# Kernel tuning notes

Hardware: AMD Instinct MI355X
Metric: run time of the kernel (lower is better)

Reference implementation:

```python
import jax, jax.numpy as jnp
import numpy as np

N_LOC = 20000
N_EXP = 200000
H = 64
E = 1500000
L = 400000


def setup_inputs() -> dict:
    key = jax.random.key(0)
    ks = jax.random.split(key, 24)
    f = jnp.float32
    w = lambda k, shp: jax.random.normal(k, shp, dtype=f) * 0.1
    # edges: ('location','of','experts'): src in [0,N_LOC), dst in [0,N_EXP)
    src = jax.random.randint(ks[0], (E,), 0, N_LOC)
    dst = jax.random.randint(ks[1], (E,), 0, N_EXP)
    edge_of = jnp.stack([src, dst])          # location -> experts
    edge_rev = jnp.stack([dst, src])         # experts -> location (ToUndirected)
    row = jax.random.randint(ks[2], (L,), 0, N_LOC)
    col = jax.random.randint(ks[3], (L,), 0, N_EXP)
    edge_label_index = jnp.stack([row, col])
    return dict(
        emb_loc=w(ks[4], (N_LOC, H)), emb_exp=w(ks[5], (N_EXP, H)),
        W1l_of=w(ks[6], (H, H)), b1_of=jnp.zeros((H,), f), W1r_of=w(ks[7], (H, H)),
        W1l_rev=w(ks[8], (H, H)), b1_rev=jnp.zeros((H,), f), W1r_rev=w(ks[9], (H, H)),
        W2l_of=w(ks[10], (H, H)), b2_of=jnp.zeros((H,), f), W2r_of=w(ks[11], (H, H)),
        W2l_rev=w(ks[12], (H, H)), b2_rev=jnp.zeros((H,), f), W2r_rev=w(ks[13], (H, H)),
        dW1=w(ks[14], (2 * H, H)), db1=jnp.zeros((H,), f),
        dW2=w(ks[15], (H, 1)), db2=jnp.zeros((1,), f),
        edge_of=edge_of, edge_rev=edge_rev, edge_label_index=edge_label_index,
    )


def _sage(x_src, x_dst, edge, Wl, b, Wr, n_dst):
    # PyG SAGEConv: lin_l(mean of neighbor msgs) + lin_r(x_dst); bias only in lin_l
    s, d = edge[0], edge[1]
    msg = x_src[s]                                   # [E, H] gather
    summed = jax.ops.segment_sum(msg, d, num_segments=n_dst)
    cnt = jax.ops.segment_sum(jnp.ones((edge.shape[1],), x_src.dtype), d, num_segments=n_dst)
    agg = summed / jnp.maximum(cnt, 1.0)[:, None]
    return agg @ Wl + b + x_dst @ Wr


def reference(emb_loc, emb_exp,
              W1l_of, b1_of, W1r_of, W1l_rev, b1_rev, W1r_rev,
              W2l_of, b2_of, W2r_of, W2l_rev, b2_rev, W2r_rev,
              dW1, db1, dW2, db2,
              edge_of, edge_rev, edge_label_index):
    # layer 1 (to_hetero: one conv per edge type; each dst type has one incoming type)
    z_exp = jax.nn.relu(_sage(emb_loc, emb_exp, edge_of, W1l_of, b1_of, W1r_of, N_EXP))
    z_loc = jax.nn.relu(_sage(emb_exp, emb_loc, edge_rev, W1l_rev, b1_rev, W1r_rev, N_LOC))
    # layer 2 (no relu)
    z_exp2 = _sage(z_loc, z_exp, edge_of, W2l_of, b2_of, W2r_of, N_EXP)
    z_loc2 = _sage(z_exp, z_loc, edge_rev, W2l_rev, b2_rev, W2r_rev, N_LOC)
    # EdgeDecoder: gather-concat-MLP
    row, col = edge_label_index[0], edge_label_index[1]
    z = jnp.concatenate([z_loc2[row], z_exp2[col]], axis=-1)  # [L, 2H]
    h = jax.nn.relu(z @ dW1 + db1)
    out = (h @ dW2 + db2).reshape(-1)
    return out
```

## Files before the change

### kernel.cpp

```cpp
#include <hip/hip_runtime.h>

#define H 64
#define NE 1500000
#define NLOC 20000
#define NEXP 200000
#define NL 400000
#define PAD_E 32
#define PAD_L 128

#define EB 896
#define NBE 224
#define LB 112
#define NBL 179
#define BIN_CHUNK 2048
#define NBIN ((NE + BIN_CHUNK - 1) / BIN_CHUNK)
#define EBSLOT 28
#define LBSLOT 32
#define ECAP 8192
#define LCAP 10240
#define FCAP 4096

#define WS_NEED 90546112ULL

typedef int vint4 __attribute__((ext_vector_type(4)));
typedef _Float16 f16x8 __attribute__((ext_vector_type(8)));
typedef float f32x4 __attribute__((ext_vector_type(4)));
typedef unsigned int u32;
typedef unsigned short u16;
typedef unsigned long long u64;

__device__ __forceinline__ float bcastf(float v, int k) {
  return __int_as_float(__builtin_amdgcn_readlane(__float_as_int(v), k));
}
__device__ __forceinline__ int bcasti(int v, int k) {
  return __builtin_amdgcn_readlane(v, k);
}

__global__ __launch_bounds__(256) void bin_kernel(
    const int* __restrict__ src, const int* __restrict__ dst,
    u32* __restrict__ expQ, u32* __restrict__ locQ,
    int* __restrict__ qcnt, int* __restrict__ flbk_cnt,
    u64* __restrict__ flbkQ)
{
  __shared__ u32 eb[NBE * EBSLOT];
  __shared__ u32 lb[NBL * LBSLOT];
  __shared__ int ec[NBE], lc[NBL], ebase[NBE], lbase[NBL];

  const int tid = threadIdx.x;
  for (int i = tid; i < NBE; i += 256) ec[i] = 0;
  for (int i = tid; i < NBL; i += 256) lc[i] = 0;
  __syncthreads();

  const long base = (long)blockIdx.x * BIN_CHUNK + tid * 8;
  if (base < NE) {
    vint4 s0 = __builtin_nontemporal_load((const vint4*)(src + base));
    vint4 s1 = __builtin_nontemporal_load((const vint4*)(src + base + 4));
    vint4 d0 = __builtin_nontemporal_load((const vint4*)(dst + base));
    vint4 d1 = __builtin_nontemporal_load((const vint4*)(dst + base + 4));
    int ss[8] = {s0.x, s0.y, s0.z, s0.w, s1.x, s1.y, s1.z, s1.w};
    int dd[8] = {d0.x, d0.y, d0.z, d0.w, d1.x, d1.y, d1.z, d1.w};
#pragma unroll
    for (int k = 0; k < 8; k++) {
      const u32 d = (u32)dd[k], s = (u32)ss[k];
      {
        const u32 b = d / (u32)EB;
        const int pos = atomicAdd(&ec[b], 1);
        if (pos < EBSLOT) {
          eb[b * EBSLOT + pos] = ((d - b * EB) << 16) | s;
        } else {
          int fi = atomicAdd(flbk_cnt, 1);
          if (fi < FCAP) flbkQ[fi] = ((u64)d << 32) | (u64)s;
        }
      }
      {
        const u32 b = s / (u32)LB;
        const int pos = atomicAdd(&lc[b], 1);
        if (pos < LBSLOT) {
          lb[b * LBSLOT + pos] = ((s - b * LB) << 18) | d;
        } else {
          int fi = atomicAdd(flbk_cnt, 1);
          if (fi < FCAP) flbkQ[fi] = (1ULL << 63) | ((u64)s << 32) | (u64)d;
        }
      }
    }
  }
  __syncthreads();

  for (int i = tid; i < NBE; i += 256) {
    const int c = min(ec[i], EBSLOT);
    ebase[i] = c ? atomicAdd(&qcnt[i], c) : 0;
  }
  for (int i = tid; i < NBL; i += 256) {
    const int c = min(lc[i], LBSLOT);
    lbase[i] = c ? atomicAdd(&qcnt[NBE + i], c) : 0;
  }
  __syncthreads();

  const int wid = tid >> 6, ln = tid & 63;
  for (int b = wid; b < NBE; b += 4) {
    const int c = min(ec[b], EBSLOT);
    if (ln < c) {
      const int idx = ebase[b] + ln;
      const u32 r = eb[b * EBSLOT + ln];
      if (idx < ECAP) {
        expQ[(long)b * ECAP + idx] = r;
      } else {
        int fi = atomicAdd(flbk_cnt, 1);
        if (fi < FCAP)
          flbkQ[fi] = ((u64)(b * EB + (r >> 16)) << 32) | (u64)(r & 0xFFFF);
      }
    }
  }
  for (int b = wid; b < NBL; b += 4) {
    const int c = min(lc[b], LBSLOT);
    if (ln < c) {
      const int idx = lbase[b] + ln;
      const u32 r = lb[b * LBSLOT + ln];
      if (idx < LCAP) {
        locQ[(long)b * LCAP + idx] = r;
      } else {
        int fi = atomicAdd(flbk_cnt, 1);
        if (fi < FCAP)
          flbkQ[fi] = (1ULL << 63) | ((u64)(b * LB + (r >> 18)) << 32) |
                      (u64)(r & 0x3FFFF);
      }
    }
  }
}

__global__ __launch_bounds__(256) void build_kernel(
    const u32* __restrict__ expQ, const u32* __restrict__ locQ,
    const int* __restrict__ qcnt,
    u16* __restrict__ nbr_exp, int* __restrict__ nbr_loc,
    int* __restrict__ cnt_exp, int* __restrict__ cnt_loc)
{
  __shared__ char ldsraw[60928];
  const int tid = threadIdx.x;
  if (blockIdx.x < NBE) {
    const int b = blockIdx.x;
    u16* rows = (u16*)ldsraw;
    int* cnts = (int*)(ldsraw + 57344);
    for (int i = tid; i < EB; i += 256) cnts[i] = 0;
    __syncthreads();
    const int n = min(qcnt[b], ECAP);
    for (int i = tid; i < n; i += 256) {
      const u32 r = expQ[(long)b * ECAP + i];
      const int nl = (int)(r >> 16);
      const int pos = atomicAdd(&cnts[nl], 1);
      if (pos < PAD_E) rows[nl * PAD_E + pos] = (u16)(r & 0xFFFF);
    }
    __syncthreads();
    const int node0 = b * EB;
    const int nn = min(EB, NEXP - node0);
    u32* grows = (u32*)(nbr_exp + (long)node0 * PAD_E);
    const u32* lrows = (const u32*)rows;
    for (int j = tid; j < nn * (PAD_E / 2); j += 256) grows[j] = lrows[j];
    for (int i = tid; i < nn; i += 256) cnt_exp[node0 + i] = cnts[i];
  } else {
    const int b = blockIdx.x - NBE;
    int* rows = (int*)ldsraw;
    int* cnts = (int*)(ldsraw + 57344);
    for (int i = tid; i < LB; i += 256) cnts[i] = 0;
    __syncthreads();
    const int n = min(qcnt[NBE + b], LCAP);
    for (int i = tid; i < n; i += 256) {
      const u32 r = locQ[(long)b * LCAP + i];
      const int sl = (int)(r >> 18);
      const int pos = atomicAdd(&cnts[sl], 1);
      if (pos < PAD_L) rows[sl * PAD_L + pos] = (int)(r & 0x3FFFF);
    }
    __syncthreads();
    const int node0 = b * LB;
    const int nn = min(LB, NLOC - node0);
    int* grows = nbr_loc + (long)node0 * PAD_L;
    for (int j = tid; j < nn * PAD_L; j += 256) grows[j] = rows[j];
    for (int i = tid; i < nn; i += 256) cnt_loc[node0 + i] = cnts[i];
  }
}

__global__ __launch_bounds__(256) void prep_kernel(
    const float* __restrict__ W2r_of, const float* __restrict__ W2l_of,
    const float* __restrict__ W2l_rev, const float* __restrict__ W2r_rev,
    const float* __restrict__ dW1, const float* __restrict__ b2_of,
    const float* __restrict__ b2_rev,
    float* __restrict__ Wf_q, float* __restrict__ Wf_y2,
    float* __restrict__ Wf_t2, float* __restrict__ Wf_p,
    float* __restrict__ bf_q, float* __restrict__ bf_p,
    const int* __restrict__ flbk_cnt, const u64* __restrict__ flbkQ,
    u16* __restrict__ nbr_exp, int* __restrict__ nbr_loc,
    int* __restrict__ cnt_exp, int* __restrict__ cnt_loc,
    const float* __restrict__ emb_loc, _Float16* __restrict__ Ylh,
    const float* __restrict__ W1l_of)
{
  const int lane = threadIdx.x & 63;
  const int w = threadIdx.x >> 6;
  const float* dW1a = dW1;
  const float* dW1b = dW1 + H * H;
  if (blockIdx.x < 4) {
    const float* A; const float* B; float* C;
    switch (blockIdx.x) {
      case 0:  A = W2r_of;  B = dW1b; C = Wf_q;  break;
      case 1:  A = W2l_of;  B = dW1b; C = Wf_y2; break;
      case 2:  A = W2l_rev; B = dW1a; C = Wf_t2; break;
      default: A = W2r_rev; B = dW1a; C = Wf_p;  break;
    }
    float b[H];
#pragma unroll
    for (int k = 0; k < H; k++) b[k] = B[k * H + lane];
    for (int r = w * 16; r < w * 16 + 16; r++) {
      const float xv = A[r * H + lane];
      float a0 = 0.f, a1 = 0.f;
#pragma unroll
      for (int k = 0; k < H; k += 2) {
        a0 += bcastf(xv, k)     * b[k];
        a1 += bcastf(xv, k + 1) * b[k + 1];
      }
      C[r * H + lane] = a0 + a1;
    }
  } else if (blockIdx.x == 4) {
    if (w < 2) {
      const float* bv_src = (w == 0) ? b2_of : b2_rev;
      const float* B      = (w == 0) ? dW1b  : dW1a;
      float* o            = (w == 0) ? bf_q  : bf_p;
      float wk[H];
#pragma unroll
      for (int k = 0; k < H; k++) wk[k] = B[k * H + lane];
      const float bv = bv_src[lane];
      float a = 0.f;
#pragma unroll
      for (int k = 0; k < H; k++) a += bcastf(bv, k) * wk[k];
      o[lane] = a;
    }
  } else if (blockIdx.x == 5) {
    const int n = min(*flbk_cnt, FCAP);
    for (int i = threadIdx.x; i < n; i += 256) {
      const u64 rec = flbkQ[i];
      const int node = (int)((rec >> 32) & 0x3FFFF);
      const int val  = (int)(rec & 0x3FFFF);
      if ((rec >> 63) == 0) {
        int pos = atomicAdd(&cnt_exp[node], 1);
        if (pos < PAD_E) nbr_exp[(long)node * PAD_E + pos] = (u16)val;
      } else {
        int pos = atomicAdd(&cnt_loc[node], 1);
        if (pos < PAD_L) nbr_loc[(long)node * PAD_L + pos] = val;
      }
    }
  } else {
    float wreg[H];
#pragma unroll
    for (int k = 0; k < H; k++) wreg[k] = W1l_of[k * H + lane];
    const int gw2 = (blockIdx.x - 6) * 4 + w;
    for (int r = gw2; r < NLOC; r += 5000) {
      const float xv = emb_loc[(long)r * H + lane];
      float a0 = 0.f, a1 = 0.f;
#pragma unroll
      for (int k = 0; k < H; k += 2) {
        a0 += bcastf(xv, k)     * wreg[k];
        a1 += bcastf(xv, k + 1) * wreg[k + 1];
      }
      Ylh[(long)r * H + lane] = (_Float16)(a0 + a1);
    }
  }
}

__global__ __launch_bounds__(256, 4) void dense_linear_kernel(
    const float* __restrict__ x, _Float16* __restrict__ out16,
    const float* __restrict__ W, int n)
{
  const int lane = threadIdx.x & 63;
  const int gw = (blockIdx.x * 256 + threadIdx.x) >> 6;
  const int nw = (gridDim.x * 256) >> 6;
  float w[H];
#pragma unroll
  for (int k = 0; k < H; k++) w[k] = W[k * H + lane];
  for (int i = gw; i < n; i += nw) {
    const float xv = x[i * H + lane];
    float a0 = 0.f, a1 = 0.f;
#pragma unroll
    for (int k = 0; k < H; k += 2) {
      a0 += bcastf(xv, k)     * w[k];
      a1 += bcastf(xv, k + 1) * w[k + 1];
    }
    out16[i * H + lane] = (_Float16)(a0 + a1);
  }
}

__global__ __launch_bounds__(256, 4) void mfma_pass_kernel(
    const u16* __restrict__ nbr, const int* __restrict__ cnt,
    const _Float16* __restrict__ y,
    const float* a32, const _Float16* a16,
    _Float16* out1, const float* __restrict__ W1,
    const float* __restrict__ bias, int relu,
    _Float16* out2, const float* __restrict__ W2)
{
  const int w = threadIdx.x >> 6;
  const int lane = threadIdx.x & 63;
  const int q = lane >> 4;
  const int cidx = lane & 15;
  const int rb = blockIdx.x * 16;

  __shared__ float Gs[16 * 68];

  f16x8 b1lo, b1hi, b2lo, b2hi;
#pragma unroll
  for (int j = 0; j < 8; j++) {
    b1lo[j] = (_Float16)W1[(q * 8 + j) * H + w * 16 + cidx];
    b1hi[j] = (_Float16)W1[(32 + q * 8 + j) * H + w * 16 + cidx];
  }
  if (out2) {
#pragma unroll
    for (int j = 0; j < 8; j++) {
      b2lo[j] = (_Float16)W2[(q * 8 + j) * H + w * 16 + cidx];
      b2hi[j] = (_Float16)W2[(32 + q * 8 + j) * H + w * 16 + cidx];
    }
  }

  f16x8 a0, a1;
  if (a16) {
    const _Float16* ar = a16 + (long)(rb + cidx) * H;
    a0 = *(const f16x8*)(ar + q * 8);
    a1 = *(const f16x8*)(ar + 32 + q * 8);
  } else {
    const float* ar = a32 + (long)(rb + cidx) * H;
    f32x4 v0 = *(const f32x4*)(ar + q * 8);
    f32x4 v1 = *(const f32x4*)(ar + q * 8 + 4);
    f32x4 v2 = *(const f32x4*)(ar + 32 + q * 8);
    f32x4 v3 = *(const f32x4*)(ar + 32 + q * 8 + 4);
#pragma unroll
    for (int j = 0; j < 4; j++) {
      a0[j] = (_Float16)v0[j];
      a0[j + 4] = (_Float16)v1[j];
      a1[j] = (_Float16)v2[j];
      a1[j + 4] = (_Float16)v3[j];
    }
  }

  if (y) {
    const int i0r = rb + w * 4;
    int c4[4];
#pragma unroll
    for (int rr = 0; rr < 4; rr++) c4[rr] = cnt[i0r + rr];
    int id4[4];
#pragma unroll
    for (int rr = 0; rr < 4; rr++) {
      const int c = min(c4[rr], PAD_E);
      id4[rr] = (lane < c) ? (int)nbr[(long)(i0r + rr) * PAD_E + lane] : 0;
    }
#pragma unroll
    for (int rr = 0; rr < 4; rr++) {
      const int cc = min(c4[rr], PAD_E);
      const int id = id4[rr];
      float s0 = 0.f, s1 = 0.f, s2 = 0.f, s3 = 0.f;
      int k = 0;
      const int m4 = cc & ~3;
      for (; k < m4; k += 4) {
        const int i0 = bcasti(id, k), i1 = bcasti(id, k + 1),
                  i2 = bcasti(id, k + 2), i3 = bcasti(id, k + 3);
        s0 += (float)y[(long)i0 * H + lane];
        s1 += (float)y[(long)i1 * H + lane];
        s2 += (float)y[(long)i2 * H + lane];
        s3 += (float)y[(long)i3 * H + lane];
      }
      for (; k < cc; k++) s0 += (float)y[(long)bcasti(id, k) * H + lane];
      Gs[(w * 4 + rr) * 68 + lane] =
          ((s0 + s1) + (s2 + s3)) / fmaxf((float)c4[rr], 1.0f);
    }
  }

  f32x4 acc1 = {0.f, 0.f, 0.f, 0.f};
  acc1 = __builtin_amdgcn_mfma_f32_16x16x32_f16(a0, b1lo, acc1, 0, 0, 0);
  acc1 = __builtin_amdgcn_mfma_f32_16x16x32_f16(a1, b1hi, acc1, 0, 0, 0);
  f32x4 acc2 = {0.f, 0.f, 0.f, 0.f};
  if (out2) {
    acc2 = __builtin_amdgcn_mfma_f32_16x16x32_f16(a0, b2lo, acc2, 0, 0, 0);
    acc2 = __builtin_amdgcn_mfma_f32_16x16x32_f16(a1, b2hi, acc2, 0, 0, 0);
  }

  const float bj = bias ? bias[w * 16 + cidx] : 0.f;
  __syncthreads();
#pragma unroll
  for (int reg = 0; reg < 4; reg++) {
    const int r = q * 4 + reg;
    float v = acc1[reg] + bj;
    if (y) v += Gs[r * 68 + w * 16 + cidx];
    if (relu) v = fmaxf(v, 0.f);
    out1[(long)(rb + r) * H + w * 16 + cidx] = (_Float16)v;
    if (out2)
      out2[(long)(rb + r) * H + w * 16 + cidx] = (_Float16)acc2[reg];
  }
}

__global__ __launch_bounds__(256, 4) void loc_gather_kernel(
    const int* __restrict__ nbr, const int* __restrict__ cnt,
    const _Float16* __restrict__ T, const float* __restrict__ x,
    float* __restrict__ out32, _Float16* __restrict__ out16,
    const float* __restrict__ Wr, const float* __restrict__ bias,
    int n, int relu)
{
  const int lane = threadIdx.x & 63;
  const int gw = (blockIdx.x * 256 + threadIdx.x) >> 6;
  const int nw = (gridDim.x * 256) >> 6;
  float wr[H];
#pragma unroll
  for (int k = 0; k < H; k++) wr[k] = Wr[k * H + lane];
  const float bj = bias[lane];
  for (int i = gw; i < n; i += nw) {
    const int c = cnt[i];
    const int cc = min(c, PAD_L);
    const int* nb = nbr + (long)i * PAD_L;
    float s0 = 0.f, s1 = 0.f, s2 = 0.f, s3 = 0.f;
    float s4 = 0.f, s5 = 0.f, s6 = 0.f, s7 = 0.f;
    int e = 0;
    while (e < cc) {
      const int m = min(cc - e, 64);
      const int id = (lane < m) ? nb[e + lane] : 0;
      int k = 0;
      const int m8 = m & ~7;
      for (; k < m8; k += 8) {
        const int i0 = bcasti(id, k),     i1 = bcasti(id, k + 1),
                  i2 = bcasti(id, k + 2), i3 = bcasti(id, k + 3),
                  i4 = bcasti(id, k + 4), i5 = bcasti(id, k + 5),
                  i6 = bcasti(id, k + 6), i7 = bcasti(id, k + 7);
        s0 += (float)T[(long)i0 * H + lane];
        s1 += (float)T[(long)i1 * H + lane];
        s2 += (float)T[(long)i2 * H + lane];
        s3 += (float)T[(long)i3 * H + lane];
        s4 += (float)T[(long)i4 * H + lane];
        s5 += (float)T[(long)i5 * H + lane];
        s6 += (float)T[(long)i6 * H + lane];
        s7 += (float)T[(long)i7 * H + lane];
      }
      const int m4 = m & ~3;
      for (; k < m4; k += 4) {
        const int i0 = bcasti(id, k), i1 = bcasti(id, k + 1),
                  i2 = bcasti(id, k + 2), i3 = bcasti(id, k + 3);
        s0 += (float)T[(long)i0 * H + lane];
        s1 += (float)T[(long)i1 * H + lane];
        s2 += (float)T[(long)i2 * H + lane];
        s3 += (float)T[(long)i3 * H + lane];
      }
      for (; k < m; k++) s0 += (float)T[(long)bcasti(id, k) * H + lane];
      e += m;
    }
    const float agg = (((s0 + s1) + (s2 + s3)) + ((s4 + s5) + (s6 + s7))) /
                      fmaxf((float)c, 1.0f);
    const float xv = x[(long)i * H + lane];
    float a0 = 0.f, a1 = 0.f;
#pragma unroll
    for (int k = 0; k < H; k += 2) {
      a0 += bcastf(xv, k)     * wr[k];
      a1 += bcastf(xv, k + 1) * wr[k + 1];
    }
    float acc = agg + bj + a0 + a1;
    if (relu) acc = fmaxf(acc, 0.0f);
    if (out32) out32[(long)i * H + lane] = acc;
    else       out16[(long)i * H + lane] = (_Float16)acc;
  }
}

__global__ __launch_bounds__(256, 4) void edge_kernel(
    const int* __restrict__ row, const int* __restrict__ col,
    const _Float16* __restrict__ P, const _Float16* __restrict__ Q,
    const float* __restrict__ db1, const float* __restrict__ dW2,
    const float* __restrict__ db2, float* __restrict__ out)
{
  const int lane = threadIdx.x & 63;
  const int gw = (blockIdx.x * 256 + threadIdx.x) >> 6;
  const int nw = (gridDim.x * 256) >> 6;
  const float bj = db1[lane];
  const float w2 = dW2[lane];
  const float b2 = db2[0];
  for (int e = gw * 4; e < NL; e += nw * 4) {
    const int n4 = min(NL - e, 4);
    float h[4];
#pragma unroll
    for (int k = 0; k < 4; k++) {
      if (k < n4) {
        const int r = row[e + k], c = col[e + k];
        const float p = (float)P[(long)r * H + lane];
        const float q = (float)Q[(long)c * H + lane];
        h[k] = fmaxf(p + q + bj, 0.0f) * w2;
      } else h[k] = 0.f;
    }
#pragma unroll
    for (int off = 1; off < 64; off <<= 1) {
#pragma unroll
      for (int k = 0; k < 4; k++) h[k] += __shfl_xor(h[k], off);
    }
    if (lane == 0) {
#pragma unroll
      for (int k = 0; k < 4; k++)
        if (k < n4) out[e + k] = h[k] + b2;
    }
  }
}

extern "C" void kernel_launch(void* const* d_in, const int* in_sizes, int n_in,
                              void* d_out, int out_size, void* d_ws, size_t ws_size,
                              hipStream_t stream) {
  const float* emb_loc = (const float*)d_in[0];
  const float* emb_exp = (const float*)d_in[1];
  const float* W1l_of  = (const float*)d_in[2];
  const float* b1_of   = (const float*)d_in[3];
  const float* W1r_of  = (const float*)d_in[4];
  const float* W1l_rev = (const float*)d_in[5];
  const float* b1_rev  = (const float*)d_in[6];
  const float* W1r_rev = (const float*)d_in[7];
  const float* W2l_of  = (const float*)d_in[8];
  const float* b2_of   = (const float*)d_in[9];
  const float* W2r_of  = (const float*)d_in[10];
  const float* W2l_rev = (const float*)d_in[11];
  const float* b2_rev  = (const float*)d_in[12];
  const float* W2r_rev = (const float*)d_in[13];
  const float* dW1     = (const float*)d_in[14];
  const float* db1     = (const float*)d_in[15];
  const float* dW2     = (const float*)d_in[16];
  const float* db2     = (const float*)d_in[17];
  const int*   edge_of = (const int*)d_in[18];
  const int*   eli     = (const int*)d_in[20];

  const int* src = edge_of;
  const int* dst = edge_of + NE;
  const int* row = eli;
  const int* col = eli + NL;

  if (ws_size < WS_NEED) return;

  char* ws = (char*)d_ws;
  int*            cnt_loc = (int*)(ws);
  int*            cnt_exp = (int*)(ws + 80000);
  int*            nbr_loc = (int*)(ws + 880064);
  unsigned short* nbr_exp = (unsigned short*)(ws + 11120064);
  _Float16*       Ylh     = (_Float16*)(ws + 23920064);
  _Float16*       Y2fh    = (_Float16*)(ws + 26480064);
  float*          z_loc   = (float*)(ws + 29040064);
  _Float16*       PH      = (_Float16*)(ws + 34160064);
  _Float16*       ZE      = (_Float16*)(ws + 39280064);
  _Float16*       TH      = (_Float16*)(ws + 64880064);
  u32*            expQ    = (u32*)(ws + 64880064);
  u32*            locQ    = (u32*)(ws + 72220096);
  int*            qcnt    = (int*)(ws + 79551936);
  int*            flbk    = (int*)(ws + 79553552);
  u64*            flbkQ   = (u64*)(ws + 79554048);
  float*          Wf_q    = (float*)(ws + 90480064);
  float*          Wf_y2   = (float*)(ws + 90496448);
  float*          Wf_t2   = (float*)(ws + 90512832);
  float*          Wf_p    = (float*)(ws + 90529216);
  float*          bf_q    = (float*)(ws + 90545600);
  float*          bf_p    = (float*)(ws + 90545856);
  float*          out     = (float*)d_out;

  (void)hipMemsetAsync(ws + 79551936, 0, 2048, stream);

  bin_kernel<<<NBIN, 256, 0, stream>>>(src, dst, expQ, locQ, qcnt, flbk, flbkQ);
  build_kernel<<<NBE + NBL, 256, 0, stream>>>(expQ, locQ, qcnt,
      nbr_exp, nbr_loc, cnt_exp, cnt_loc);
  prep_kernel<<<1256, 256, 0, stream>>>(W2r_of, W2l_of, W2l_rev, W2r_rev,
                                        dW1, b2_of, b2_rev,
                                        Wf_q, Wf_y2, Wf_t2, Wf_p, bf_q, bf_p,
                                        flbk, flbkQ, nbr_exp, nbr_loc,
                                        cnt_exp, cnt_loc,
                                        emb_loc, Ylh, W1l_of);

  mfma_pass_kernel<<<NEXP / 16, 256, 0, stream>>>(nbr_exp, cnt_exp, Ylh,
      emb_exp, (const _Float16*)nullptr, ZE, W1r_of, b1_of, 1, TH, W1l_rev);
  loc_gather_kernel<<<2048, 256, 0, stream>>>(nbr_loc, cnt_loc, TH,
      emb_loc, z_loc, (_Float16*)nullptr, W1r_rev, b1_rev, NLOC, 1);

  dense_linear_kernel<<<1280, 256, 0, stream>>>(z_loc, Y2fh, Wf_y2, NLOC);
  mfma_pass_kernel<<<NEXP / 16, 256, 0, stream>>>(nbr_exp, cnt_exp, Y2fh,
      (const float*)nullptr, ZE, ZE, Wf_q, bf_q, 0, TH, Wf_t2);
  loc_gather_kernel<<<2048, 256, 0, stream>>>(nbr_loc, cnt_loc, TH,
      z_loc, (float*)nullptr, PH, Wf_p, bf_p, NLOC, 0);

  edge_kernel<<<2048, 256, 0, stream>>>(row, col, PH, ZE,
                                        db1, dW2, db2, out);
}
```

Baseline: 513.1 us.

## Vectorize fp16 row gathers four-rows-per-wave and pretranspose fp16 MFMA weights

The neighbour-gather loops in the mfma pass, the loc gather and the edge decoder now fetch four rows per wave instruction. Each 16-lane group loads an f16x4 slice of a different neighbour row, and the partial sums are reduced with cross-lane shuffles. This replaces per-lane 2-byte loads of one row at a time. Weight operands for the MFMA kernel are pre-transposed to fp16 in the prep kernel so the B fragments load as contiguous f16x8 vectors instead of strided scalar reads. The change adds masking, lane-select and shuffle overhead, and it relies on clamping indices to valid neighbours for the padded lanes.

```diff
diff --git a/kernel.cpp b/kernel.cpp
--- a/kernel.cpp
+++ b/kernel.cpp
@@ -24,6 +24,7 @@
 
 typedef int vint4 __attribute__((ext_vector_type(4)));
 typedef _Float16 f16x8 __attribute__((ext_vector_type(8)));
+typedef _Float16 f16x4 __attribute__((ext_vector_type(4)));
 typedef float f32x4 __attribute__((ext_vector_type(4)));
 typedef unsigned int u32;
 typedef unsigned short u16;
@@ -34,6 +35,9 @@
 }
 __device__ __forceinline__ int bcasti(int v, int k) {
   return __builtin_amdgcn_readlane(v, k);
+}
+__device__ __forceinline__ int sel4(int g, int n0, int n1, int n2, int n3) {
+  return (g & 2) ? ((g & 1) ? n3 : n2) : ((g & 1) ? n1 : n0);
 }
 
 __global__ __launch_bounds__(256) void bin_kernel(
@@ -190,19 +194,22 @@
     u16* __restrict__ nbr_exp, int* __restrict__ nbr_loc,
     int* __restrict__ cnt_exp, int* __restrict__ cnt_loc,
     const float* __restrict__ emb_loc, _Float16* __restrict__ Ylh,
-    const float* __restrict__ W1l_of)
+    const float* __restrict__ W1l_of,
+    const float* __restrict__ W1r_of, const float* __restrict__ W1l_rev,
+    _Float16* __restrict__ W1rT16, _Float16* __restrict__ W1lrT16,
+    _Float16* __restrict__ WfqT16, _Float16* __restrict__ Wft2T16)
 {
   const int lane = threadIdx.x & 63;
   const int w = threadIdx.x >> 6;
   const float* dW1a = dW1;
   const float* dW1b = dW1 + H * H;
   if (blockIdx.x < 4) {
-    const float* A; const float* B; float* C;
+    const float* A; const float* B; float* C; _Float16* CT;
     switch (blockIdx.x) {
-      case 0:  A = W2r_of;  B = dW1b; C = Wf_q;  break;
-      case 1:  A = W2l_of;  B = dW1b; C = Wf_y2; break;
-      case 2:  A = W2l_rev; B = dW1a; C = Wf_t2; break;
-      default: A = W2r_rev; B = dW1a; C = Wf_p;  break;
+      case 0:  A = W2r_of;  B = dW1b; C = Wf_q;  CT = WfqT16;  break;
+      case 1:  A = W2l_of;  B = dW1b; C = Wf_y2; CT = nullptr; break;
+      case 2:  A = W2l_rev; B = dW1a; C = Wf_t2; CT = Wft2T16; break;
+      default: A = W2r_rev; B = dW1a; C = Wf_p;  CT = nullptr; break;
     }
     float b[H];
 #pragma unroll
@@ -215,7 +222,9 @@
         a0 += bcastf(xv, k)     * b[k];
         a1 += bcastf(xv, k + 1) * b[k + 1];
       }
-      C[r * H + lane] = a0 + a1;
+      const float val = a0 + a1;
+      C[r * H + lane] = val;
+      if (CT) CT[(long)lane * H + r] = (_Float16)val;
     }
   } else if (blockIdx.x == 4) {
     if (w < 2) {
@@ -245,11 +254,16 @@
         if (pos < PAD_L) nbr_loc[(long)node * PAD_L + pos] = val;
       }
     }
+  } else if (blockIdx.x < 8) {
+    const float* S = (blockIdx.x == 6) ? W1r_of : W1l_rev;
+    _Float16* D    = (blockIdx.x == 6) ? W1rT16 : W1lrT16;
+    for (int k = w * 16; k < w * 16 + 16; k++)
+      D[(long)lane * H + k] = (_Float16)S[(long)k * H + lane];
   } else {
     float wreg[H];
 #pragma unroll
     for (int k = 0; k < H; k++) wreg[k] = W1l_of[k * H + lane];
-    const int gw2 = (blockIdx.x - 6) * 4 + w;
+    const int gw2 = (blockIdx.x - 8) * 4 + w;
     for (int r = gw2; r < NLOC; r += 5000) {
       const float xv = emb_loc[(long)r * H + lane];
       float a0 = 0.f, a1 = 0.f;
@@ -289,9 +303,9 @@
     const u16* __restrict__ nbr, const int* __restrict__ cnt,
     const _Float16* __restrict__ y,
     const float* a32, const _Float16* a16,
-    _Float16* out1, const float* __restrict__ W1,
+    _Float16* out1, const _Float16* __restrict__ W1T,
     const float* __restrict__ bias, int relu,
-    _Float16* out2, const float* __restrict__ W2)
+    _Float16* out2, const _Float16* __restrict__ W2T)
 {
   const int w = threadIdx.x >> 6;
   const int lane = threadIdx.x & 63;
@@ -301,18 +315,14 @@
 
   __shared__ float Gs[16 * 68];
 
-  f16x8 b1lo, b1hi, b2lo, b2hi;
-#pragma unroll
-  for (int j = 0; j < 8; j++) {
-    b1lo[j] = (_Float16)W1[(q * 8 + j) * H + w * 16 + cidx];
-    b1hi[j] = (_Float16)W1[(32 + q * 8 + j) * H + w * 16 + cidx];
-  }
+  const _Float16* bt1 = W1T + (long)(w * 16 + cidx) * H;
+  f16x8 b1lo = *(const f16x8*)(bt1 + q * 8);
+  f16x8 b1hi = *(const f16x8*)(bt1 + 32 + q * 8);
+  f16x8 b2lo, b2hi;
   if (out2) {
-#pragma unroll
-    for (int j = 0; j < 8; j++) {
-      b2lo[j] = (_Float16)W2[(q * 8 + j) * H + w * 16 + cidx];
-      b2hi[j] = (_Float16)W2[(32 + q * 8 + j) * H + w * 16 + cidx];
-    }
+    const _Float16* bt2 = W2T + (long)(w * 16 + cidx) * H;
+    b2lo = *(const f16x8*)(bt2 + q * 8);
+    b2hi = *(const f16x8*)(bt2 + 32 + q * 8);
   }
 
   f16x8 a0, a1;
@@ -337,33 +347,46 @@
 
   if (y) {
     const int i0r = rb + w * 4;
-    int c4[4];
-#pragma unroll
-    for (int rr = 0; rr < 4; rr++) c4[rr] = cnt[i0r + rr];
+    const int g = lane >> 4;
+    const int sub = lane & 15;
+    int c4v[4];
+#pragma unroll
+    for (int rr = 0; rr < 4; rr++) c4v[rr] = cnt[i0r + rr];
     int id4[4];
 #pragma unroll
     for (int rr = 0; rr < 4; rr++) {
-      const int c = min(c4[rr], PAD_E);
+      const int c = min(c4v[rr], PAD_E);
       id4[rr] = (lane < c) ? (int)nbr[(long)(i0r + rr) * PAD_E + lane] : 0;
     }
 #pragma unroll
     for (int rr = 0; rr < 4; rr++) {
-      const int cc = min(c4[rr], PAD_E);
+      const int cc = min(c4v[rr], PAD_E);
       const int id = id4[rr];
+      const int kl = cc - 1;
       float s0 = 0.f, s1 = 0.f, s2 = 0.f, s3 = 0.f;
-      int k = 0;
-      const int m4 = cc & ~3;
-      for (; k < m4; k += 4) {
-        const int i0 = bcasti(id, k), i1 = bcasti(id, k + 1),
-                  i2 = bcasti(id, k + 2), i3 = bcasti(id, k + 3);
-        s0 += (float)y[(long)i0 * H + lane];
-        s1 += (float)y[(long)i1 * H + lane];
-        s2 += (float)y[(long)i2 * H + lane];
-        s3 += (float)y[(long)i3 * H + lane];
-      }
-      for (; k < cc; k++) s0 += (float)y[(long)bcasti(id, k) * H + lane];
-      Gs[(w * 4 + rr) * 68 + lane] =
-          ((s0 + s1) + (s2 + s3)) / fmaxf((float)c4[rr], 1.0f);
+      for (int k = 0; k < cc; k += 4) {
+        const int n0 = bcasti(id, k);
+        const int n1 = bcasti(id, min(k + 1, kl));
+        const int n2 = bcasti(id, min(k + 2, kl));
+        const int n3 = bcasti(id, min(k + 3, kl));
+        const int ns = sel4(g, n0, n1, n2, n3);
+        const f16x4 v = *(const f16x4*)(y + (long)ns * H + sub * 4);
+        const float msk = (k + g < cc) ? 1.0f : 0.0f;
+        s0 = fmaf(msk, (float)v[0], s0);
+        s1 = fmaf(msk, (float)v[1], s1);
+        s2 = fmaf(msk, (float)v[2], s2);
+        s3 = fmaf(msk, (float)v[3], s3);
+      }
+      s0 += __shfl_xor(s0, 16); s0 += __shfl_xor(s0, 32);
+      s1 += __shfl_xor(s1, 16); s1 += __shfl_xor(s1, 32);
+      s2 += __shfl_xor(s2, 16); s2 += __shfl_xor(s2, 32);
+      s3 += __shfl_xor(s3, 16); s3 += __shfl_xor(s3, 32);
+      const float inv = 1.0f / fmaxf((float)c4v[rr], 1.0f);
+      if (lane < 16) {
+        float* gp = &Gs[(w * 4 + rr) * 68 + 4 * lane];
+        gp[0] = s0 * inv; gp[1] = s1 * inv;
+        gp[2] = s2 * inv; gp[3] = s3 * inv;
+      }
     }
   }
 
@@ -400,6 +423,8 @@
   const int lane = threadIdx.x & 63;
   const int gw = (blockIdx.x * 256 + threadIdx.x) >> 6;
   const int nw = (gridDim.x * 256) >> 6;
+  const int g = lane >> 4;
+  const int sub = lane & 15;
   float wr[H];
 #pragma unroll
   for (int k = 0; k < H; k++) wr[k] = Wr[k * H + lane];
@@ -414,36 +439,46 @@
     while (e < cc) {
       const int m = min(cc - e, 64);
       const int id = (lane < m) ? nb[e + lane] : 0;
-      int k = 0;
-      const int m8 = m & ~7;
-      for (; k < m8; k += 8) {
-        const int i0 = bcasti(id, k),     i1 = bcasti(id, k + 1),
-                  i2 = bcasti(id, k + 2), i3 = bcasti(id, k + 3),
-                  i4 = bcasti(id, k + 4), i5 = bcasti(id, k + 5),
-                  i6 = bcasti(id, k + 6), i7 = bcasti(id, k + 7);
-        s0 += (float)T[(long)i0 * H + lane];
-        s1 += (float)T[(long)i1 * H + lane];
-        s2 += (float)T[(long)i2 * H + lane];
-        s3 += (float)T[(long)i3 * H + lane];
-        s4 += (float)T[(long)i4 * H + lane];
-        s5 += (float)T[(long)i5 * H + lane];
-        s6 += (float)T[(long)i6 * H + lane];
-        s7 += (float)T[(long)i7 * H + lane];
-      }
-      const int m4 = m & ~3;
-      for (; k < m4; k += 4) {
-        const int i0 = bcasti(id, k), i1 = bcasti(id, k + 1),
-                  i2 = bcasti(id, k + 2), i3 = bcasti(id, k + 3);
-        s0 += (float)T[(long)i0 * H + lane];
-        s1 += (float)T[(long)i1 * H + lane];
-        s2 += (float)T[(long)i2 * H + lane];
-        s3 += (float)T[(long)i3 * H + lane];
-      }
-      for (; k < m; k++) s0 += (float)T[(long)bcasti(id, k) * H + lane];
+      const int ml = m - 1;
+      for (int k = 0; k < m; k += 8) {
+        const int a0i = bcasti(id, k);
+        const int a1i = bcasti(id, min(k + 1, ml));
+        const int a2i = bcasti(id, min(k + 2, ml));
+        const int a3i = bcasti(id, min(k + 3, ml));
+        const int nsA = sel4(g, a0i, a1i, a2i, a3i);
+        const f16x4 vA = *(const f16x4*)(T + (long)nsA * H + sub * 4);
+        const int b0i = bcasti(id, min(k + 4, ml));
+        const int b1i = bcasti(id, min(k + 5, ml));
+        const int b2i = bcasti(id, min(k + 6, ml));
+        const int b3i = bcasti(id, min(k + 7, ml));
+        const int nsB = sel4(g, b0i, b1i, b2i, b3i);
+        const f16x4 vB = *(const f16x4*)(T + (long)nsB * H + sub * 4);
+        const float mA = (k + g < m) ? 1.0f : 0.0f;
+        const float mB = (k + 4 + g < m) ? 1.0f : 0.0f;
+        s0 = fmaf(mA, (float)vA[0], s0);
+        s1 = fmaf(mA, (float)vA[1], s1);
+        s2 = fmaf(mA, (float)vA[2], s2);
+        s3 = fmaf(mA, (float)vA[3], s3);
+        s4 = fmaf(mB, (float)vB[0], s4);
+        s5 = fmaf(mB, (float)vB[1], s5);
+        s6 = fmaf(mB, (float)vB[2], s6);
+        s7 = fmaf(mB, (float)vB[3], s7);
+      }
       e += m;
     }
-    const float agg = (((s0 + s1) + (s2 + s3)) + ((s4 + s5) + (s6 + s7))) /
-                      fmaxf((float)c, 1.0f);
+    s0 += s4; s1 += s5; s2 += s6; s3 += s7;
+    s0 += __shfl_xor(s0, 16); s0 += __shfl_xor(s0, 32);
+    s1 += __shfl_xor(s1, 16); s1 += __shfl_xor(s1, 32);
+    s2 += __shfl_xor(s2, 16); s2 += __shfl_xor(s2, 32);
+    s3 += __shfl_xor(s3, 16); s3 += __shfl_xor(s3, 32);
+    const int srcl = lane >> 2;
+    const float v0 = __shfl(s0, srcl);
+    const float v1 = __shfl(s1, srcl);
+    const float v2 = __shfl(s2, srcl);
+    const float v3 = __shfl(s3, srcl);
+    const int r2 = lane & 3;
+    const float sg = (r2 & 2) ? ((r2 & 1) ? v3 : v2) : ((r2 & 1) ? v1 : v0);
+    const float agg = sg / fmaxf((float)c, 1.0f);
     const float xv = x[(long)i * H + lane];
     float a0 = 0.f, a1 = 0.f;
 #pragma unroll
@@ -467,31 +502,27 @@
   const int lane = threadIdx.x & 63;
   const int gw = (blockIdx.x * 256 + threadIdx.x) >> 6;
   const int nw = (gridDim.x * 256) >> 6;
-  const float bj = db1[lane];
-  const float w2 = dW2[lane];
+  const int g = lane >> 4;
+  const int sub = lane & 15;
+  const f32x4 bj4 = *(const f32x4*)(db1 + 4 * sub);
+  const f32x4 w24 = *(const f32x4*)(dW2 + 4 * sub);
   const float b2 = db2[0];
   for (int e = gw * 4; e < NL; e += nw * 4) {
-    const int n4 = min(NL - e, 4);
-    float h[4];
-#pragma unroll
-    for (int k = 0; k < 4; k++) {
-      if (k < n4) {
-        const int r = row[e + k], c = col[e + k];
-        const float p = (float)P[(long)r * H + lane];
-        const float q = (float)Q[(long)c * H + lane];
-        h[k] = fmaxf(p + q + bj, 0.0f) * w2;
-      } else h[k] = 0.f;
-    }
-#pragma unroll
-    for (int off = 1; off < 64; off <<= 1) {
-#pragma unroll
-      for (int k = 0; k < 4; k++) h[k] += __shfl_xor(h[k], off);
-    }
-    if (lane == 0) {
-#pragma unroll
-      for (int k = 0; k < 4; k++)
-        if (k < n4) out[e + k] = h[k] + b2;
-    }
+    const int r0 = row[e], r1 = row[e + 1], r2i = row[e + 2], r3 = row[e + 3];
+    const int c0 = col[e], c1 = col[e + 1], c2i = col[e + 2], c3 = col[e + 3];
+    const int rs = sel4(g, r0, r1, r2i, r3);
+    const int cs = sel4(g, c0, c1, c2i, c3);
+    const f16x4 pv = *(const f16x4*)(P + (long)rs * H + sub * 4);
+    const f16x4 qv = *(const f16x4*)(Q + (long)cs * H + sub * 4);
+    float h = fmaxf((float)pv[0] + (float)qv[0] + bj4[0], 0.f) * w24[0]
+            + fmaxf((float)pv[1] + (float)qv[1] + bj4[1], 0.f) * w24[1]
+            + fmaxf((float)pv[2] + (float)qv[2] + bj4[2], 0.f) * w24[2]
+            + fmaxf((float)pv[3] + (float)qv[3] + bj4[3], 0.f) * w24[3];
+    h += __shfl_xor(h, 1);
+    h += __shfl_xor(h, 2);
+    h += __shfl_xor(h, 4);
+    h += __shfl_xor(h, 8);
+    if (sub == 0) out[e + g] = h + b2;
   }
 }
 
@@ -535,6 +566,10 @@
   _Float16*       Y2fh    = (_Float16*)(ws + 26480064);
   float*          z_loc   = (float*)(ws + 29040064);
   _Float16*       PH      = (_Float16*)(ws + 34160064);
+  _Float16*       W1rT16  = (_Float16*)(ws + 36720064);
+  _Float16*       W1lrT16 = (_Float16*)(ws + 36728256);
+  _Float16*       WfqT16  = (_Float16*)(ws + 36736448);
+  _Float16*       Wft2T16 = (_Float16*)(ws + 36744640);
   _Float16*       ZE      = (_Float16*)(ws + 39280064);
   _Float16*       TH      = (_Float16*)(ws + 64880064);
   u32*            expQ    = (u32*)(ws + 64880064);
@@ -555,21 +590,23 @@
   bin_kernel<<<NBIN, 256, 0, stream>>>(src, dst, expQ, locQ, qcnt, flbk, flbkQ);
   build_kernel<<<NBE + NBL, 256, 0, stream>>>(expQ, locQ, qcnt,
       nbr_exp, nbr_loc, cnt_exp, cnt_loc);
-  prep_kernel<<<1256, 256, 0, stream>>>(W2r_of, W2l_of, W2l_rev, W2r_rev,
+  prep_kernel<<<1258, 256, 0, stream>>>(W2r_of, W2l_of, W2l_rev, W2r_rev,
                                         dW1, b2_of, b2_rev,
                                         Wf_q, Wf_y2, Wf_t2, Wf_p, bf_q, bf_p,
                                         flbk, flbkQ, nbr_exp, nbr_loc,
                                         cnt_exp, cnt_loc,
-                                        emb_loc, Ylh, W1l_of);
+                                        emb_loc, Ylh, W1l_of,
+                                        W1r_of, W1l_rev,
+                                        W1rT16, W1lrT16, WfqT16, Wft2T16);
 
   mfma_pass_kernel<<<NEXP / 16, 256, 0, stream>>>(nbr_exp, cnt_exp, Ylh,
-      emb_exp, (const _Float16*)nullptr, ZE, W1r_of, b1_of, 1, TH, W1l_rev);
+      emb_exp, (const _Float16*)nullptr, ZE, W1rT16, b1_of, 1, TH, W1lrT16);
   loc_gather_kernel<<<2048, 256, 0, stream>>>(nbr_loc, cnt_loc, TH,
       emb_loc, z_loc, (_Float16*)nullptr, W1r_rev, b1_rev, NLOC, 1);
 
   dense_linear_kernel<<<1280, 256, 0, stream>>>(z_loc, Y2fh, Wf_y2, NLOC);
   mfma_pass_kernel<<<NEXP / 16, 256, 0, stream>>>(nbr_exp, cnt_exp, Y2fh,
-      (const float*)nullptr, ZE, ZE, Wf_q, bf_q, 0, TH, Wf_t2);
+      (const float*)nullptr, ZE, ZE, WfqT16, bf_q, 0, TH, Wft2T16);
   loc_gather_kernel<<<2048, 256, 0, stream>>>(nbr_loc, cnt_loc, TH,
       z_loc, (float*)nullptr, PH, Wf_p, bf_p, NLOC, 0);
 
```

Result: faster. 501.5 us, median of 2 (-2.3%).
